# Performance work log

Hardware: AMD Instinct MI355X
Metric: run time of the kernel (lower is better)

The kernel has to match this reference:

```python
import jax, jax.numpy as jnp
import numpy as np


def setup_inputs() -> dict:
    key = jax.random.key(0)
    k1, k2, k3 = jax.random.split(key, 3)
    B, C, D, H, W = 4, 64, 32, 64, 64
    x = jax.random.normal(k1, (B, C, D, H, W), dtype=jnp.float32)
    # Conv3d(in=2, out=1, k=7), PyTorch default init: U(-s, s), s = 1/sqrt(fan_in)
    fan_in = 2 * 7 * 7 * 7
    s = 1.0 / np.sqrt(fan_in)
    conv_w = jax.random.uniform(k2, (1, 2, 7, 7, 7), dtype=jnp.float32, minval=-s, maxval=s)
    conv_b = jax.random.uniform(k3, (1,), dtype=jnp.float32, minval=-s, maxval=s)
    return {"x": x, "conv_w": conv_w, "conv_b": conv_b}


def reference(x, conv_w, conv_b):
    # channel-wise max and mean -> [B, 2, D, H, W]
    xc = jnp.stack([jnp.max(x, axis=1), jnp.mean(x, axis=1)], axis=1)
    # conv3d 2->1, k7, stride 1, padding 3 (SAME)
    y = jax.lax.conv_general_dilated(
        xc, conv_w,
        window_strides=(1, 1, 1),
        padding=[(3, 3), (3, 3), (3, 3)],
        dimension_numbers=("NCDHW", "OIDHW", "NCDHW"),
    ) + conv_b[None, :, None, None, None]
    scale = jax.nn.sigmoid(y)  # [B, 1, D, H, W]
    return x * scale
```

## Files before the change

### kernel.cpp

```cpp
#include <hip/hip_runtime.h>
#include <math.h>

#define B_ 4
#define C_ 64
#define D_ 32
#define H_ 64
#define W_ 64
#define S_ (D_*H_*W_)
#define S4_ (S_/4)

typedef float floatx4 __attribute__((ext_vector_type(4)));

__global__ __launch_bounds__(256) void reduce_kernel(const float* __restrict__ x,
                                                     float* __restrict__ xc) {
    int i  = blockIdx.x * 256 + threadIdx.x;
    int b  = i >> 15;
    int s4 = i & (S4_ - 1);
    const float4* x4 = reinterpret_cast<const float4*>(x) + (size_t)b * C_ * S4_ + s4;
    float4 v = x4[0];
    float mx0 = v.x, mx1 = v.y, mx2 = v.z, mx3 = v.w;
    float sm0 = v.x, sm1 = v.y, sm2 = v.z, sm3 = v.w;
    #pragma unroll 8
    for (int c = 1; c < C_; ++c) {
        float4 t = x4[(size_t)c * S4_];
        mx0 = fmaxf(mx0, t.x); sm0 += t.x;
        mx1 = fmaxf(mx1, t.y); sm1 += t.y;
        mx2 = fmaxf(mx2, t.z); sm2 += t.z;
        mx3 = fmaxf(mx3, t.w); sm3 += t.w;
    }
    float4* o = reinterpret_cast<float4*>(xc);
    float4 a; a.x = mx0; a.y = mx1; a.z = mx2; a.w = mx3;
    o[((size_t)b * 2 + 0) * S4_ + s4] = a;
    const float inv = 1.0f / 64.0f;
    float4 m; m.x = sm0 * inv; m.y = sm1 * inv; m.z = sm2 * inv; m.w = sm3 * inv;
    o[((size_t)b * 2 + 1) * S4_ + s4] = m;
}

#define HX 44
#define HY 14
#define HZ 10
#define HROW (HY*HX)
__global__ __launch_bounds__(256) void conv_gate_kernel(const float* __restrict__ xc,
                                                        const float* __restrict__ x,
                                                        const float* __restrict__ cw,
                                                        const float* __restrict__ cb,
                                                        float* __restrict__ out) {
    __shared__ float tile[HZ * HROW];
    __shared__ float wl[392];

    const int tid = threadIdx.x;
    const int b  = blockIdx.z >> 3;
    const int d0 = (blockIdx.z & 7) * 4;
    const int h0 = blockIdx.y * 8;
    const int w0 = blockIdx.x * 32;

    const int wg = tid & 7;
    const int hg = (tid >> 3) & 7;
    const int dz = tid >> 6;

    float acc0 = 0.f, acc1 = 0.f, acc2 = 0.f, acc3 = 0.f;

    for (int ch = 0; ch < 2; ++ch) {
        for (int idx = tid; idx < 392; idx += 256) {
            int kz = idx / 56;
            int r  = idx - kz * 56;
            int ky = r >> 3;
            int kw = r & 7;
            wl[idx] = (kw < 7) ? cw[ch * 343 + kz * 49 + ky * 7 + kw] : 0.f;
        }
        for (int idx = tid; idx < HZ * HY * 38; idx += 256) {
            int z = idx / (HY * 38);
            int r = idx - z * (HY * 38);
            int y = r / 38;
            int xw = r - y * 38;
            int gd = d0 + z - 3, gh = h0 + y - 3, gw = w0 + xw - 3;
            float v = 0.f;
            if ((unsigned)gd < (unsigned)D_ && (unsigned)gh < (unsigned)H_ &&
                (unsigned)gw < (unsigned)W_)
                v = xc[((size_t)(b * 2 + ch)) * S_ + gd * (H_ * W_) + gh * W_ + gw];
            tile[z * HROW + y * HX + xw] = v;
        }
        __syncthreads();

        for (int kz = 0; kz < 7; ++kz) {
            const float* base = &tile[(dz + kz) * HROW + hg * HX + wg * 4];
            #pragma unroll
            for (int ky = 0; ky < 7; ++ky) {
                float4 f0 = *reinterpret_cast<const float4*>(base + ky * HX);
                float4 f1 = *reinterpret_cast<const float4*>(base + ky * HX + 4);
                float2 f2 = *reinterpret_cast<const float2*>(base + ky * HX + 8);
                float win[10] = {f0.x, f0.y, f0.z, f0.w, f1.x, f1.y, f1.z, f1.w, f2.x, f2.y};
                const float* wr = &wl[kz * 56 + ky * 8];
                float4 wa = *reinterpret_cast<const float4*>(wr);
                float4 wb = *reinterpret_cast<const float4*>(wr + 4);
                float wt[7] = {wa.x, wa.y, wa.z, wa.w, wb.x, wb.y, wb.z};
                #pragma unroll
                for (int kw = 0; kw < 7; ++kw) {
                    acc0 = fmaf(win[kw + 0], wt[kw], acc0);
                    acc1 = fmaf(win[kw + 1], wt[kw], acc1);
                    acc2 = fmaf(win[kw + 2], wt[kw], acc2);
                    acc3 = fmaf(win[kw + 3], wt[kw], acc3);
                }
            }
        }
        __syncthreads();
    }

    const float bias = cb[0];
    floatx4 s0;
    s0.x = 1.0f / (1.0f + __expf(-(acc0 + bias)));
    s0.y = 1.0f / (1.0f + __expf(-(acc1 + bias)));
    s0.z = 1.0f / (1.0f + __expf(-(acc2 + bias)));
    s0.w = 1.0f / (1.0f + __expf(-(acc3 + bias)));

    const int d = d0 + dz, h = h0 + hg, w = w0 + wg * 4;
    const size_t sp = (size_t)d * (H_ * W_) + (size_t)h * W_ + w;
    const float* xp = x + (size_t)b * C_ * S_ + sp;
    float* op = out + (size_t)b * C_ * S_ + sp;
    #pragma unroll 8
    for (int c = 0; c < C_; ++c) {
        const size_t off = (size_t)c * S_;
        floatx4 xv = *reinterpret_cast<const floatx4*>(xp + off);
        __builtin_nontemporal_store(xv * s0, reinterpret_cast<floatx4*>(op + off));
    }
}

extern "C" void kernel_launch(void* const* d_in, const int* in_sizes, int n_in,
                              void* d_out, int out_size, void* d_ws, size_t ws_size,
                              hipStream_t stream) {
    const float* x  = (const float*)d_in[0];
    const float* cw = (const float*)d_in[1];
    const float* cb = (const float*)d_in[2];
    float* out = (float*)d_out;
    float* xc  = (float*)d_ws;

    reduce_kernel<<<dim3((B_ * S4_) / 256), dim3(256), 0, stream>>>(x, xc);
    conv_gate_kernel<<<dim3(W_ / 32, H_ / 8, B_ * (D_ / 4)), dim3(256), 0, stream>>>(
        xc, x, cw, cb, out);
}
```

Baseline: 96.45 us.

## Retile conv-gate to full-width rows and load both channels before one barrier

```diff
diff --git a/kernel.cpp b/kernel.cpp
--- a/kernel.cpp
+++ b/kernel.cpp
@@ -36,61 +36,62 @@
     o[((size_t)b * 2 + 1) * S4_ + s4] = m;
 }
 
-#define HX 44
-#define HY 14
-#define HZ 10
-#define HROW (HY*HX)
+#define YS 72
+#define ZS (10*YS)
+#define CHS (10*ZS)
 __global__ __launch_bounds__(256) void conv_gate_kernel(const float* __restrict__ xc,
                                                         const float* __restrict__ x,
                                                         const float* __restrict__ cw,
                                                         const float* __restrict__ cb,
                                                         float* __restrict__ out) {
-    __shared__ float tile[HZ * HROW];
-    __shared__ float wl[392];
+    __shared__ float tile[2 * CHS];
+    __shared__ float wl[784];
 
     const int tid = threadIdx.x;
     const int b  = blockIdx.z >> 3;
     const int d0 = (blockIdx.z & 7) * 4;
-    const int h0 = blockIdx.y * 8;
-    const int w0 = blockIdx.x * 32;
+    const int h0 = blockIdx.y * 4;
 
-    const int wg = tid & 7;
-    const int hg = (tid >> 3) & 7;
-    const int dz = tid >> 6;
+    const int w4 = tid & 15;
+    const int hh = (tid >> 4) & 3;
+    const int dd = tid >> 6;
+
+    for (int idx = tid; idx < 784; idx += 256) {
+        int ch = idx / 392;
+        int r  = idx - ch * 392;
+        int kz = r / 56;
+        int r2 = r - kz * 56;
+        int ky = r2 >> 3;
+        int kw = r2 & 7;
+        wl[idx] = (kw < 7) ? cw[ch * 343 + kz * 49 + ky * 7 + kw] : 0.f;
+    }
+    for (int idx = tid; idx < 2 * 10 * 10 * 70; idx += 256) {
+        int ch = idx / 7000;
+        int r  = idx - ch * 7000;
+        int z  = r / 700;
+        int r2 = r - z * 700;
+        int y  = r2 / 70;
+        int xw = r2 - y * 70;
+        int gd = d0 + z - 3, gh = h0 + y - 3, gw = xw - 3;
+        float v = 0.f;
+        if ((unsigned)gd < (unsigned)D_ && (unsigned)gh < (unsigned)H_ &&
+            (unsigned)gw < (unsigned)W_)
+            v = xc[((size_t)(b * 2 + ch)) * S_ + gd * (H_ * W_) + gh * W_ + gw];
+        tile[ch * CHS + z * ZS + y * YS + xw] = v;
+    }
+    __syncthreads();
 
     float acc0 = 0.f, acc1 = 0.f, acc2 = 0.f, acc3 = 0.f;
-
     for (int ch = 0; ch < 2; ++ch) {
-        for (int idx = tid; idx < 392; idx += 256) {
-            int kz = idx / 56;
-            int r  = idx - kz * 56;
-            int ky = r >> 3;
-            int kw = r & 7;
-            wl[idx] = (kw < 7) ? cw[ch * 343 + kz * 49 + ky * 7 + kw] : 0.f;
-        }
-        for (int idx = tid; idx < HZ * HY * 38; idx += 256) {
-            int z = idx / (HY * 38);
-            int r = idx - z * (HY * 38);
-            int y = r / 38;
-            int xw = r - y * 38;
-            int gd = d0 + z - 3, gh = h0 + y - 3, gw = w0 + xw - 3;
-            float v = 0.f;
-            if ((unsigned)gd < (unsigned)D_ && (unsigned)gh < (unsigned)H_ &&
-                (unsigned)gw < (unsigned)W_)
-                v = xc[((size_t)(b * 2 + ch)) * S_ + gd * (H_ * W_) + gh * W_ + gw];
-            tile[z * HROW + y * HX + xw] = v;
-        }
-        __syncthreads();
-
         for (int kz = 0; kz < 7; ++kz) {
-            const float* base = &tile[(dz + kz) * HROW + hg * HX + wg * 4];
+            const float* base = &tile[ch * CHS + (dd + kz) * ZS + hh * YS + w4 * 4];
             #pragma unroll
             for (int ky = 0; ky < 7; ++ky) {
-                float4 f0 = *reinterpret_cast<const float4*>(base + ky * HX);
-                float4 f1 = *reinterpret_cast<const float4*>(base + ky * HX + 4);
-                float2 f2 = *reinterpret_cast<const float2*>(base + ky * HX + 8);
+                float4 f0 = *reinterpret_cast<const float4*>(base + ky * YS);
+                float4 f1 = *reinterpret_cast<const float4*>(base + ky * YS + 4);
+                float2 f2 = *reinterpret_cast<const float2*>(base + ky * YS + 8);
                 float win[10] = {f0.x, f0.y, f0.z, f0.w, f1.x, f1.y, f1.z, f1.w, f2.x, f2.y};
-                const float* wr = &wl[kz * 56 + ky * 8];
+                const float* wr = &wl[ch * 392 + kz * 56 + ky * 8];
                 float4 wa = *reinterpret_cast<const float4*>(wr);
                 float4 wb = *reinterpret_cast<const float4*>(wr + 4);
                 float wt[7] = {wa.x, wa.y, wa.z, wa.w, wb.x, wb.y, wb.z};
@@ -103,7 +104,6 @@
                 }
             }
         }
-        __syncthreads();
     }
 
     const float bias = cb[0];
@@ -113,7 +113,7 @@
     s0.z = 1.0f / (1.0f + __expf(-(acc2 + bias)));
     s0.w = 1.0f / (1.0f + __expf(-(acc3 + bias)));
 
-    const int d = d0 + dz, h = h0 + hg, w = w0 + wg * 4;
+    const int d = d0 + dd, h = h0 + hh, w = w4 * 4;
     const size_t sp = (size_t)d * (H_ * W_) + (size_t)h * W_ + w;
     const float* xp = x + (size_t)b * C_ * S_ + sp;
     float* op = out + (size_t)b * C_ * S_ + sp;
@@ -121,7 +121,7 @@
     for (int c = 0; c < C_; ++c) {
         const size_t off = (size_t)c * S_;
         floatx4 xv = *reinterpret_cast<const floatx4*>(xp + off);
-        __builtin_nontemporal_store(xv * s0, reinterpret_cast<floatx4*>(op + off));
+        *reinterpret_cast<floatx4*>(op + off) = xv * s0;
     }
 }
 
@@ -135,6 +135,6 @@
     float* xc  = (float*)d_ws;
 
     reduce_kernel<<<dim3((B_ * S4_) / 256), dim3(256), 0, stream>>>(x, xc);
-    conv_gate_kernel<<<dim3(W_ / 32, H_ / 8, B_ * (D_ / 4)), dim3(256), 0, stream>>>(
+    conv_gate_kernel<<<dim3(1, H_ / 4, B_ * (D_ / 4)), dim3(256), 0, stream>>>(
         xc, x, cw, cb, out);
 }
```

Result: faster. 93.54 us (-3.0%).
